# Performance work log

Measured on AMD Instinct MI355X. Metric: run time of the kernel, lower is better.

## Reference

```python
import jax, jax.numpy as jnp
import numpy as np

B, L, C, H = 4, 2048, 1024, 16
D = C // H            # head_dim = 64
TAU = 4
SCALE = 1.0 / np.sqrt(D) / TAU  # cos_attn=False path


def setup_inputs() -> dict:
    key = jax.random.key(0)
    ks = jax.random.split(key, 7)
    std = 1.0 / np.sqrt(C)
    return {
        "x": jax.random.normal(ks[0], (B, L, C), dtype=jnp.float32),
        "attn_bias": jax.random.normal(ks[1], (1, 1, L, L), dtype=jnp.float32) * 0.02,
        "W_qkv": jax.random.normal(ks[2], (3 * C, C), dtype=jnp.float32) * std,
        "q_bias": jax.random.normal(ks[3], (C,), dtype=jnp.float32) * 0.02,
        "v_bias": jax.random.normal(ks[4], (C,), dtype=jnp.float32) * 0.02,
        "W_proj": jax.random.normal(ks[5], (C, C), dtype=jnp.float32) * std,
        "b_proj": jax.random.normal(ks[6], (C,), dtype=jnp.float32) * 0.02,
    }


def reference(x, attn_bias, W_qkv, q_bias, v_bias, W_proj, b_proj):
    # qkv projection with bias = cat(q_bias, zeros_k, v_bias)
    bias = jnp.concatenate([q_bias, jnp.zeros_like(q_bias), v_bias])
    qkv = x @ W_qkv.T + bias                      # [B, L, 3C]
    qkv = qkv.reshape(B, L, 3, H, D)
    q, k, v = jnp.moveaxis(qkv, 2, 0)             # each [B, L, H, D]
    q = q.transpose(0, 2, 1, 3)                   # [B, H, L, D]
    k = k.transpose(0, 2, 1, 3)
    v = v.transpose(0, 2, 1, 3)
    # slow_attn: (q*scale) @ k^T + bias -> softmax -> @ v
    scores = jnp.einsum("bhqd,bhkd->bhqk", q * SCALE, k) + attn_bias
    attn = jax.nn.softmax(scores, axis=-1)
    oup = jnp.einsum("bhqk,bhkd->bhqd", attn, v)  # [B, H, L, D]
    oup = oup.transpose(0, 2, 1, 3).reshape(B, L, C)
    return oup @ W_proj.T + b_proj
```

## Files before the change

kernel.cpp:

```cpp
#include <hip/hip_runtime.h>
#include <hip/hip_bf16.h>

typedef unsigned short u16;
typedef unsigned int   u32;

using f32x4  = __attribute__((ext_vector_type(4)))  float;
using f32x16 = __attribute__((ext_vector_type(16))) float;
using s16x8  = __attribute__((ext_vector_type(8)))  short;
using b16x8  = __attribute__((ext_vector_type(8)))  __bf16;
using u32x4  = __attribute__((ext_vector_type(4)))  u32;

#define LOG2E 1.44269504088896f
#define QSC   (0.03125f * LOG2E)

__device__ __forceinline__ f32x4 mfma16(s16x8 a, s16x8 b, f32x4 c) {
  return __builtin_amdgcn_mfma_f32_16x16x32_bf16(
      __builtin_bit_cast(b16x8, a), __builtin_bit_cast(b16x8, b), c, 0, 0, 0);
}
__device__ __forceinline__ f32x16 mfma32(s16x8 a, s16x8 b, f32x16 c) {
  return __builtin_amdgcn_mfma_f32_32x32x16_bf16(
      __builtin_bit_cast(b16x8, a), __builtin_bit_cast(b16x8, b), c, 0, 0, 0);
}

__device__ __forceinline__ u16 f2bf(float f) {
  u32 u = __builtin_bit_cast(u32, f);
  u = (u + 0x7FFFu + ((u >> 16) & 1u)) >> 16;
  return (u16)u;
}
__device__ __forceinline__ float exp2_hw(float x) {
  float r;
  asm("v_exp_f32 %0, %1" : "=v"(r) : "v"(x));
  return r;
}
__device__ __forceinline__ u32 cvtpk(float a, float b) {
  u32 r;
  asm("v_cvt_pk_bf16_f32 %0, %1, %2" : "=v"(r) : "v"(a), "v"(b));
  return r;
}

__device__ __forceinline__ void gload16(const void* g, void* l) {
  __builtin_amdgcn_global_load_lds(
      (const __attribute__((address_space(1))) u32*)g,
      (__attribute__((address_space(3))) u32*)l, 16, 0, 0);
}

__global__ void prep(const float* __restrict__ x, const float* __restrict__ wqkv,
                     const float* __restrict__ wproj, u16* __restrict__ outc,
                     const float* __restrict__ ab, u16* __restrict__ biasr) {
  __shared__ u16 T[32][72];
  if (blockIdx.x < 2048) {
    int i = blockIdx.x * 256 + threadIdx.x;
    const int stride = 2048 * 256;
    for (; i < 3145728; i += stride) {
      const float* src = (i < 2097152) ? x + 4 * (long)i
                       : (i < 2883584) ? wqkv + 4 * ((long)i - 2097152)
                                       : wproj + 4 * ((long)i - 2883584);
      const float4 v = *(const float4*)src;
      ushort4 o;
      o.x = f2bf(v.x); o.y = f2bf(v.y); o.z = f2bf(v.z); o.w = f2bf(v.w);
      ((ushort4*)outc)[i] = o;
    }
  } else {
    const int blk  = blockIdx.x - 2048;
    const int tid  = threadIdx.x;
    const int slot = blk >> 5;
    const int kt   = blk & 31;

    {
      const int qr = tid >> 3;
      const int fc = (tid & 7) * 8;
      const float* src = ab + (long)(slot * 32 + qr) * 2048 + kt * 64 + fc;
      const float4 a = *(const float4*)(src);
      const float4 b = *(const float4*)(src + 4);
      u16 t[8];
      t[0] = f2bf(a.x * LOG2E); t[1] = f2bf(a.y * LOG2E);
      t[2] = f2bf(a.z * LOG2E); t[3] = f2bf(a.w * LOG2E);
      t[4] = f2bf(b.x * LOG2E); t[5] = f2bf(b.y * LOG2E);
      t[6] = f2bf(b.z * LOG2E); t[7] = f2bf(b.w * LOG2E);
      *(s16x8*)&T[qr][fc] = *(s16x8*)t;
    }
    __syncthreads();

    {
      const int chunk = tid >> 6;
      const int lane  = tid & 63;
      const int q5    = lane & 31;
      const int hi    = lane >> 5;
      u16 o[8];
#pragma unroll
      for (int e = 0; e < 8; ++e) {
        const int vidx = chunk * 8 + e;
        const int kb = vidx >> 4, r = vidx & 15;
        const int key = kb * 32 + (r & 3) + 8 * (r >> 2) + 4 * hi;
        o[e] = T[q5][key];
      }
      *(s16x8*)(biasr + ((long)blk * 256 + tid) * 8) = *(s16x8*)o;
    }
  }
}

template<int EPI>
__global__ __launch_bounds__(256)
void gemm_bt(const u16* __restrict__ A, const u16* __restrict__ Bm,
             int M, int N, int K,
             const float* __restrict__ bias0, const float* __restrict__ bias1,
             u16* __restrict__ oq, u16* __restrict__ ok, u16* __restrict__ ov,
             float* __restrict__ outf)
{
  __shared__ u16 As[2][128 * 32];
  __shared__ u16 Bs[2][128 * 32];

  const int tid  = threadIdx.x;
  const int w    = tid >> 6;
  const int lane = tid & 63;
  const int lr   = lane & 15;
  const int lg   = lane >> 4;
  const int wr   = w >> 1, wc = w & 1;

  const int bm = blockIdx.y, bn = blockIdx.x;

  f32x4 acc[4][4];
#pragma unroll
  for (int i = 0; i < 4; ++i)
#pragma unroll
    for (int j = 0; j < 4; ++j) acc[i][j] = (f32x4){0.f, 0.f, 0.f, 0.f};

  const int rowA = bm * 128 + (tid >> 2);
  const int rowB = bn * 128 + (tid >> 2);
  const int colk = (tid & 3) * 8;

  const u16* ga0 = A  + (long)rowA * K + colk;
  const u16* gb0 = Bm + (long)rowB * K + colk;

  gload16(ga0,          &As[0][w * 512]);
  gload16(ga0 + 64 * K, &As[0][2048 + w * 512]);
  gload16(gb0,          &Bs[0][w * 512]);
  gload16(gb0 + 64 * K, &Bs[0][2048 + w * 512]);
  asm volatile("s_waitcnt vmcnt(0)" ::: "memory");
  __syncthreads();

  const int NT = K >> 5;
  for (int t = 0; t < NT; ++t) {
    const int cur = t & 1;
    if (t + 1 < NT) {
      const u16* ga = ga0 + (t + 1) * 32;
      const u16* gb = gb0 + (t + 1) * 32;
      gload16(ga,          &As[cur ^ 1][w * 512]);
      gload16(ga + 64 * K, &As[cur ^ 1][2048 + w * 512]);
      gload16(gb,          &Bs[cur ^ 1][w * 512]);
      gload16(gb + 64 * K, &Bs[cur ^ 1][2048 + w * 512]);
    }

    s16x8 af[4], bfr[4];
#pragma unroll
    for (int mi = 0; mi < 4; ++mi)
      af[mi] = *(const s16x8*)(&As[cur][(wr * 64 + mi * 16 + lr) * 32 + lg * 8]);
#pragma unroll
    for (int ni = 0; ni < 4; ++ni)
      bfr[ni] = *(const s16x8*)(&Bs[cur][(wc * 64 + ni * 16 + lr) * 32 + lg * 8]);
#pragma unroll
    for (int mi = 0; mi < 4; ++mi)
#pragma unroll
      for (int ni = 0; ni < 4; ++ni)
        acc[mi][ni] = mfma16(af[mi], bfr[ni], acc[mi][ni]);

    asm volatile("s_waitcnt vmcnt(0)" ::: "memory");
    __syncthreads();
  }

  const int gm0 = bm * 128 + wr * 64;
  const int gn0 = bn * 128 + wc * 64;

#pragma unroll
  for (int mi = 0; mi < 4; ++mi) {
#pragma unroll
    for (int ni = 0; ni < 4; ++ni) {
      const int col  = gn0 + ni * 16 + lr;
      const int row0 = gm0 + mi * 16 + lg * 4;
      if (EPI == 0) {
        const int which = col >> 10;
        const int cj    = col & 1023;
        const float badd = (which == 0) ? bias0[cj] : (which == 2 ? bias1[cj] : 0.f);
        const int h = cj >> 6, d = cj & 63;
#pragma unroll
        for (int r = 0; r < 4; ++r) {
          const int rowg = row0 + r;
          const int b = rowg >> 11, l = rowg & 2047;
          const int bh = b * 16 + h;
          float val = acc[mi][ni][r] + badd;
          if (which == 0) val *= QSC;
          const u16 o = f2bf(val);
          if (which == 0)      oq[(bh * 2048 + l) * 64 + d] = o;
          else if (which == 1) ok[(bh * 2048 + l) * 64 + d] = o;
          else {
            const int lp = (l & ~12) | ((l & 4) << 1) | ((l & 8) >> 1);
            ov[(bh * 64 + d) * 2048 + lp] = o;
          }
        }
      } else {
        const float badd = bias0[col];
#pragma unroll
        for (int r = 0; r < 4; ++r)
          outf[(long)(row0 + r) * N + col] = acc[mi][ni][r] + badd;
      }
    }
  }
}

__global__ __launch_bounds__(256)
void flash_attn(const u16* __restrict__ qbuf, const u16* __restrict__ kbuf,
                const u16* __restrict__ vtbuf, const u16* __restrict__ biasr,
                u16* __restrict__ oup)
{
  __shared__ u16 Ks[2][64 * 72];
  __shared__ u16 Vs[2][64 * 72];

  const int tid  = threadIdx.x;
  const int w    = tid >> 6;
  const int lane = tid & 63;
  const int lq   = lane & 31;
  const int hi   = lane >> 5;

  const int bid = blockIdx.x;
  const int swz = (bid & 7) * 128 + (bid >> 3);
  const int bh  = swz >> 4, qt2 = swz & 15;
  const long base = (long)bh * (2048 * 64);

  const int qrow = qt2 * 128 + w * 32 + lq;
  s16x8 qf[4];
  {
    const u16* qp = qbuf + base + qrow * 64 + 8 * hi;
#pragma unroll
    for (int s = 0; s < 4; ++s) qf[s] = *(const s16x8*)(qp + 16 * s);
  }

  f32x16 oacc0, oacc1;
  float lacc[8];
#pragma unroll
  for (int r = 0; r < 16; ++r) { oacc0[r] = 0.f; oacc1[r] = 0.f; }
#pragma unroll
  for (int r = 0; r < 8; ++r) lacc[r] = 0.f;

  const u16* bslice = biasr + (long)(qt2 * 4 + w) * 65536 + lane * 8;

  const int sr  = tid >> 3;
  const int scc = tid & 7;
  const u16* kg = kbuf  + base + sr * 64   + scc * 8;
  const u16* vg = vtbuf + base + sr * 2048 + scc * 8;
  const int wo0 = sr * 72 + scc * 8;
  const int wo1 = (32 + sr) * 72 + scc * 8;

  {
    const s16x8 a0 = *(const s16x8*)(kg);
    const s16x8 a1 = *(const s16x8*)(kg + 2048);
    const s16x8 b0 = *(const s16x8*)(vg);
    const s16x8 b1 = *(const s16x8*)(vg + 65536);
    *(s16x8*)(&Ks[0][wo0]) = a0;  *(s16x8*)(&Ks[0][wo1]) = a1;
    *(s16x8*)(&Vs[0][wo0]) = b0;  *(s16x8*)(&Vs[0][wo1]) = b1;
  }
  __syncthreads();

  for (int kt = 0; kt < 32; ++kt) {
    const int cur = kt & 1;

    s16x8 nk0, nk1, nv0, nv1;
    if (kt < 31) {
      const u16* kn = kg + (kt + 1) * 4096;
      const u16* vn = vg + (kt + 1) * 64;
      nk0 = *(const s16x8*)(kn);
      nk1 = *(const s16x8*)(kn + 2048);
      nv0 = *(const s16x8*)(vn);
      nv1 = *(const s16x8*)(vn + 65536);
    }

    s16x8 kf0[4], kf1[4], vf0[4], vf1[4];
    {
      const u16* kb0 = &Ks[cur][lq * 72];
      const u16* kb1 = &Ks[cur][(32 + lq) * 72];
      const u16* vb0 = &Vs[cur][lq * 72];
      const u16* vb1 = &Vs[cur][(32 + lq) * 72];
#pragma unroll
      for (int s = 0; s < 4; ++s) {
        const int off = (2 * s + hi) * 8;
        kf0[s] = *(const s16x8*)(kb0 + off);
        kf1[s] = *(const s16x8*)(kb1 + off);
        vf0[s] = *(const s16x8*)(vb0 + off);
        vf1[s] = *(const s16x8*)(vb1 + off);
      }
    }

    u32x4 bb[4];
#pragma unroll
    for (int k = 0; k < 4; ++k)
      bb[k] = *(const u32x4*)(bslice + kt * 2048 + k * 512);

    f32x16 sa0, sa1;
#pragma unroll
    for (int jw = 0; jw < 8; ++jw) {
      const u32 w0 = bb[jw >> 2][jw & 3];
      const u32 w1 = bb[2 + (jw >> 2)][jw & 3];
      sa0[2 * jw]     = __builtin_bit_cast(float, w0 << 16);
      sa0[2 * jw + 1] = __builtin_bit_cast(float, w0 & 0xFFFF0000u);
      sa1[2 * jw]     = __builtin_bit_cast(float, w1 << 16);
      sa1[2 * jw + 1] = __builtin_bit_cast(float, w1 & 0xFFFF0000u);
    }

#pragma unroll
    for (int s = 0; s < 4; ++s) sa0 = mfma32(kf0[s], qf[s], sa0);
#pragma unroll
    for (int s = 0; s < 4; ++s) sa1 = mfma32(kf1[s], qf[s], sa1);

#pragma unroll
    for (int r = 0; r < 16; ++r) {
      sa0[r] = exp2_hw(sa0[r]);
      sa1[r] = exp2_hw(sa1[r]);
    }
#pragma unroll
    for (int r = 0; r < 8; ++r)
      lacc[r] += (sa0[r] + sa0[r + 8]) + (sa1[r] + sa1[r + 8]);

    s16x8 pf[4];
#pragma unroll
    for (int ks = 0; ks < 4; ++ks) {
      const f32x16 ps = (ks & 2) ? sa1 : sa0;
      const int o = (ks & 1) * 8;
      u32x4 tt;
      tt[0] = cvtpk(ps[o + 0], ps[o + 1]);
      tt[1] = cvtpk(ps[o + 2], ps[o + 3]);
      tt[2] = cvtpk(ps[o + 4], ps[o + 5]);
      tt[3] = cvtpk(ps[o + 6], ps[o + 7]);
      pf[ks] = __builtin_bit_cast(s16x8, tt);
    }

#pragma unroll
    for (int ks = 0; ks < 4; ++ks) {
      oacc0 = mfma32(vf0[ks], pf[ks], oacc0);
      oacc1 = mfma32(vf1[ks], pf[ks], oacc1);
    }

    if (kt < 31) {
      *(s16x8*)(&Ks[cur ^ 1][wo0]) = nk0;
      *(s16x8*)(&Ks[cur ^ 1][wo1]) = nk1;
      *(s16x8*)(&Vs[cur ^ 1][wo0]) = nv0;
      *(s16x8*)(&Vs[cur ^ 1][wo1]) = nv1;
    }
    __syncthreads();
  }

  u32 (*Os)[32][33] = (u32(*)[32][33])&Ks[0][0];
  const int b = bh >> 4, h = bh & 15;
  float l = ((lacc[0] + lacc[1]) + (lacc[2] + lacc[3]))
          + ((lacc[4] + lacc[5]) + (lacc[6] + lacc[7]));
  l += __shfl_xor(l, 32, 64);
  const float inv = 1.f / l;
#pragma unroll
  for (int i = 0; i < 8; ++i) {
    const int idx = (i & 1) + 2 * hi + 4 * (i >> 1);
    Os[w][lq][idx]      = cvtpk(oacc0[2 * i] * inv, oacc0[2 * i + 1] * inv);
    Os[w][lq][idx + 16] = cvtpk(oacc1[2 * i] * inv, oacc1[2 * i + 1] * inv);
  }
  __syncthreads();
#pragma unroll
  for (int it = 0; it < 4; ++it) {
    const int q = it * 8 + (lane >> 3);
    const int c = (lane & 7) * 4;
    u32x4 v;
#pragma unroll
    for (int j = 0; j < 4; ++j) v[j] = Os[w][q][c + j];
    const long row = (long)(b * 2048 + qt2 * 128 + w * 32 + q);
    *(u32x4*)(oup + row * 1024 + h * 64 + (lane & 7) * 8) = v;
  }
}

extern "C" void kernel_launch(void* const* d_in, const int* in_sizes, int n_in,
                              void* d_out, int out_size, void* d_ws, size_t ws_size,
                              hipStream_t stream) {
  const float* x     = (const float*)d_in[0];
  const float* ab    = (const float*)d_in[1];
  const float* wqkv  = (const float*)d_in[2];
  const float* qbias = (const float*)d_in[3];
  const float* vbias = (const float*)d_in[4];
  const float* wproj = (const float*)d_in[5];
  const float* bproj = (const float*)d_in[6];
  float* out = (float*)d_out;

  char* ws = (char*)d_ws;
  if (ws_size < 83886080u) return;
  u16* xb     = (u16*)(ws);
  u16* wqkvb  = (u16*)(ws + 16777216);
  u16* wprojb = (u16*)(ws + 23068672);
  u16* biasr  = (u16*)(ws + 25165824);
  u16* qbuf   = (u16*)(ws + 33554432);
  u16* kbuf   = (u16*)(ws + 50331648);
  u16* vtbuf  = (u16*)(ws + 67108864);

  prep<<<dim3(4096), dim3(256), 0, stream>>>(x, wqkv, wproj, xb, ab, biasr);

  gemm_bt<0><<<dim3(24, 64), dim3(256), 0, stream>>>(
      xb, wqkvb, 8192, 3072, 1024, qbias, vbias, qbuf, kbuf, vtbuf, nullptr);

  flash_attn<<<dim3(1024), dim3(256), 0, stream>>>(qbuf, kbuf, vtbuf, biasr, xb);

  gemm_bt<1><<<dim3(8, 64), dim3(256), 0, stream>>>(
      xb, wprojb, 8192, 1024, 1024, bproj, nullptr, nullptr, nullptr, nullptr, out);
}
```

Baseline: 227.9 us.

## Add dedicated 256x256-tile QKV GEMM with 512 threads and staged async loads

Replaces the generic 128x128 QKV projection GEMM with a specialized kernel that uses 256x256 tiles, 8 waves, 128KB of dynamic LDS double buffering, and a phased schedule that interleaves global-to-LDS loads with MFMA work. It also applies a grouped block-index swizzle to improve L2 reuse. The aim is higher arithmetic intensity and better load/compute overlap for the largest GEMM. The cost is heavy LDS use (one block per CU), many barriers, and a reliance on gload16 and layout details that are not shown.

```diff
diff --git a/kernel.cpp b/kernel.cpp
--- a/kernel.cpp
+++ b/kernel.cpp
@@ -65,7 +65,6 @@
     const int tid  = threadIdx.x;
     const int slot = blk >> 5;
     const int kt   = blk & 31;
-
     {
       const int qr = tid >> 3;
       const int fc = (tid & 7) * 8;
@@ -80,7 +79,6 @@
       *(s16x8*)&T[qr][fc] = *(s16x8*)t;
     }
     __syncthreads();
-
     {
       const int chunk = tid >> 6;
       const int lane  = tid & 63;
@@ -99,12 +97,147 @@
   }
 }
 
+__global__ __launch_bounds__(512)
+void gemm_qkv(const u16* __restrict__ A, const u16* __restrict__ Bm,
+              const float* __restrict__ bias0, const float* __restrict__ bias1,
+              u16* __restrict__ oq, u16* __restrict__ ok, u16* __restrict__ ov)
+{
+  extern __shared__ u16 lds[];
+  u16* const Al0 = lds;
+  u16* const Al1 = lds + 16384;
+  u16* const Bl0 = lds + 32768;
+  u16* const Bl1 = lds + 49152;
+
+  const int tid  = threadIdx.x;
+  const int w    = tid >> 6;
+  const int lane = tid & 63;
+  const int lr   = lane & 15;
+  const int lg   = lane >> 4;
+  const int wr   = w >> 2, wc = w & 3;
+
+  const int bid = blockIdx.x;
+  const int swz = (bid & 7) * 48 + (bid >> 3);
+  const int bn  = swz % 12, bm = swz / 12;
+
+  const int srow = tid >> 3;
+  const int skc  = (tid & 7) * 8;
+  const u16* gA = A  + (long)(bm * 256 + srow) * 1024 + skc;
+  const u16* gB = Bm + (long)(bn * 256 + srow) * 1024 + skc;
+
+#define SA(DST, T, C) gload16(gA + (long)(C) * 65536 + (T) * 64, (DST) + (C) * 4096 + w * 512)
+#define SB(DST, T, C) gload16(gB + (long)(C) * 65536 + (T) * 64, (DST) + (C) * 4096 + w * 512)
+
+  f32x4 acc[8][4];
+#pragma unroll
+  for (int m = 0; m < 8; ++m)
+#pragma unroll
+    for (int n = 0; n < 4; ++n) acc[m][n] = (f32x4){0.f, 0.f, 0.f, 0.f};
+
+  SA(Al0, 0, 0); SA(Al0, 0, 1); SA(Al0, 0, 2); SA(Al0, 0, 3);
+  SB(Bl0, 0, 0); SB(Bl0, 0, 1); SB(Bl0, 0, 2); SB(Bl0, 0, 3);
+  SA(Al1, 1, 1); SA(Al1, 1, 3); SB(Bl1, 1, 0); SB(Bl1, 1, 1);
+  asm volatile("s_waitcnt vmcnt(4)" ::: "memory");
+  __syncthreads();
+
+  const int abase = wr * 128;
+  const int bbase = wc * 64;
+
+#define PHASE(ALD, MB, STG)                                                     \
+  {                                                                             \
+    const u16* ap0 = (ALD) + (abase + (MB) * 16 + lr) * 64 + lg * 8;            \
+    const u16* ap1 = (ALD) + (abase + (MB) * 16 + 16 + lr) * 64 + lg * 8;       \
+    const s16x8 a00 = *(const s16x8*)(ap0);                                     \
+    const s16x8 a01 = *(const s16x8*)(ap0 + 32);                                \
+    const s16x8 a10 = *(const s16x8*)(ap1);                                     \
+    const s16x8 a11 = *(const s16x8*)(ap1 + 32);                                \
+    STG;                                                                        \
+    _Pragma("unroll")                                                           \
+    for (int n = 0; n < 4; ++n) {                                               \
+      acc[MB][n]     = mfma16(a00, bf[n][0], acc[MB][n]);                       \
+      acc[MB][n]     = mfma16(a01, bf[n][1], acc[MB][n]);                       \
+      acc[MB + 1][n] = mfma16(a10, bf[n][0], acc[MB + 1][n]);                   \
+      acc[MB + 1][n] = mfma16(a11, bf[n][1], acc[MB + 1][n]);                   \
+    }                                                                           \
+  }
+
+  for (int i = 0; i < 8; ++i) {
+    const int t1 = 2 * i + 1, t2 = 2 * i + 2, t3 = 2 * i + 3;
+    s16x8 bf[4][2];
+
+#pragma unroll
+    for (int n = 0; n < 4; ++n) {
+      const u16* bp = Bl0 + (bbase + n * 16 + lr) * 64 + lg * 8;
+      bf[n][0] = *(const s16x8*)(bp);
+      bf[n][1] = *(const s16x8*)(bp + 32);
+    }
+    PHASE(Al0, 6, { SB(Bl1, t1, 2); SB(Bl1, t1, 3); SA(Al1, t1, 0); SA(Al1, t1, 2); });
+    __syncthreads();
+    PHASE(Al0, 4, {});
+    __syncthreads();
+    PHASE(Al0, 2, { if (t2 < 16) { SA(Al0, t2, 1); SA(Al0, t2, 3); } });
+    __syncthreads();
+    PHASE(Al0, 0, { if (t2 < 16) { SB(Bl0, t2, 0); SB(Bl0, t2, 1); } });
+    if (i < 7) asm volatile("s_waitcnt vmcnt(4)" ::: "memory");
+    else       asm volatile("s_waitcnt vmcnt(0)" ::: "memory");
+    __syncthreads();
+
+#pragma unroll
+    for (int n = 0; n < 4; ++n) {
+      const u16* bp = Bl1 + (bbase + n * 16 + lr) * 64 + lg * 8;
+      bf[n][0] = *(const s16x8*)(bp);
+      bf[n][1] = *(const s16x8*)(bp + 32);
+    }
+    PHASE(Al1, 6, { if (t2 < 16) { SB(Bl0, t2, 2); SB(Bl0, t2, 3); } });
+    __syncthreads();
+    PHASE(Al1, 4, { if (t2 < 16) { SA(Al0, t2, 0); SA(Al0, t2, 2); } });
+    __syncthreads();
+    PHASE(Al1, 2, { if (t3 < 16) { SA(Al1, t3, 1); SA(Al1, t3, 3); } });
+    __syncthreads();
+    PHASE(Al1, 0, { if (t3 < 16) { SB(Bl1, t3, 0); SB(Bl1, t3, 1); } });
+    if (i < 7) asm volatile("s_waitcnt vmcnt(4)" ::: "memory");
+    else       asm volatile("s_waitcnt vmcnt(0)" ::: "memory");
+    __syncthreads();
+  }
+#undef PHASE
+#undef SA
+#undef SB
+
+  const int gm0 = bm * 256 + wr * 128;
+  const int gn0 = bn * 256 + wc * 64;
+#pragma unroll
+  for (int m = 0; m < 8; ++m) {
+#pragma unroll
+    for (int n = 0; n < 4; ++n) {
+      const int col  = gn0 + n * 16 + lr;
+      const int row0 = gm0 + m * 16 + lg * 4;
+      const int which = col >> 10;
+      const int cj    = col & 1023;
+      const float badd = (which == 0) ? bias0[cj] : (which == 2 ? bias1[cj] : 0.f);
+      const int h = cj >> 6, d = cj & 63;
+#pragma unroll
+      for (int r = 0; r < 4; ++r) {
+        const int rowg = row0 + r;
+        const int b = rowg >> 11, l = rowg & 2047;
+        const int bh = b * 16 + h;
+        float val = acc[m][n][r] + badd;
+        if (which == 0) val *= QSC;
+        const u16 o = f2bf(val);
+        if (which == 0)      oq[(bh * 2048 + l) * 64 + d] = o;
+        else if (which == 1) ok[(bh * 2048 + l) * 64 + d] = o;
+        else {
+          const int lp = (l & ~12) | ((l & 4) << 1) | ((l & 8) >> 1);
+          ov[(bh * 64 + d) * 2048 + lp] = o;
+        }
+      }
+    }
+  }
+}
+
 template<int EPI>
 __global__ __launch_bounds__(256)
 void gemm_bt(const u16* __restrict__ A, const u16* __restrict__ Bm,
              int M, int N, int K,
-             const float* __restrict__ bias0, const float* __restrict__ bias1,
-             u16* __restrict__ oq, u16* __restrict__ ok, u16* __restrict__ ov,
+             const float* __restrict__ bias0,
              float* __restrict__ outf)
 {
   __shared__ u16 As[2][128 * 32];
@@ -177,32 +310,10 @@
     for (int ni = 0; ni < 4; ++ni) {
       const int col  = gn0 + ni * 16 + lr;
       const int row0 = gm0 + mi * 16 + lg * 4;
-      if (EPI == 0) {
-        const int which = col >> 10;
-        const int cj    = col & 1023;
-        const float badd = (which == 0) ? bias0[cj] : (which == 2 ? bias1[cj] : 0.f);
-        const int h = cj >> 6, d = cj & 63;
-#pragma unroll
-        for (int r = 0; r < 4; ++r) {
-          const int rowg = row0 + r;
-          const int b = rowg >> 11, l = rowg & 2047;
-          const int bh = b * 16 + h;
-          float val = acc[mi][ni][r] + badd;
-          if (which == 0) val *= QSC;
-          const u16 o = f2bf(val);
-          if (which == 0)      oq[(bh * 2048 + l) * 64 + d] = o;
-          else if (which == 1) ok[(bh * 2048 + l) * 64 + d] = o;
-          else {
-            const int lp = (l & ~12) | ((l & 4) << 1) | ((l & 8) >> 1);
-            ov[(bh * 64 + d) * 2048 + lp] = o;
-          }
-        }
-      } else {
-        const float badd = bias0[col];
-#pragma unroll
-        for (int r = 0; r < 4; ++r)
-          outf[(long)(row0 + r) * N + col] = acc[mi][ni][r] + badd;
-      }
+      const float badd = bias0[col];
+#pragma unroll
+      for (int r = 0; r < 4; ++r)
+        outf[(long)(row0 + r) * N + col] = acc[mi][ni][r] + badd;
     }
   }
 }
@@ -396,11 +507,11 @@
 
   prep<<<dim3(4096), dim3(256), 0, stream>>>(x, wqkv, wproj, xb, ab, biasr);
 
-  gemm_bt<0><<<dim3(24, 64), dim3(256), 0, stream>>>(
-      xb, wqkvb, 8192, 3072, 1024, qbias, vbias, qbuf, kbuf, vtbuf, nullptr);
+  gemm_qkv<<<dim3(384), dim3(512), 131072, stream>>>(
+      xb, wqkvb, qbias, vbias, qbuf, kbuf, vtbuf);
 
   flash_attn<<<dim3(1024), dim3(256), 0, stream>>>(qbuf, kbuf, vtbuf, biasr, xb);
 
   gemm_bt<1><<<dim3(8, 64), dim3(256), 0, stream>>>(
-      xb, wprojb, 8192, 1024, 1024, bproj, nullptr, nullptr, nullptr, nullptr, out);
-}
+      xb, wprojb, 8192, 1024, 1024, bproj, out);
+}
```

Result: slower. 271.1 us (+18.9%).
